# Optimization experiments

Hardware: AMD Instinct MI355X
Metric: run time of the kernel (lower is better)

The kernel has to match this reference:

```python
import jax, jax.numpy as jnp
import numpy as np

S = 7
B = 2
CLS = 20
N = CLS + B * 5  # 30
LAMBDA_COORD = 5.0
LAMBDA_NOOBJ = 0.5
BATCH = 16384


def setup_inputs() -> dict:
    key = jax.random.key(0)
    k1, k2, k3 = jax.random.split(key, 3)
    pred = jax.random.uniform(k1, (BATCH, S, S, N), dtype=jnp.float32)
    target = jax.random.uniform(k2, (BATCH, S, S, N), dtype=jnp.float32)
    # conf channel (index 4) must be exactly 0 or 1 -- it drives the obj/noobj masks
    obj = (jax.random.uniform(k3, (BATCH, S, S)) < 0.15).astype(jnp.float32)
    target = target.at[..., 4].set(obj)
    return {"pred": pred, "target": target}


def _iou(b1, b2):
    # b1: [M, B, 4] xyxy, b2: [M, 4] xyxy -> [M, B]
    lt = jnp.maximum(b1[..., :2], b2[:, None, :2])
    rb = jnp.minimum(b1[..., 2:], b2[:, None, 2:])
    wh = jnp.clip(rb - lt, 0.0)
    inter = wh[..., 0] * wh[..., 1]
    area1 = (b1[..., 2] - b1[..., 0]) * (b1[..., 3] - b1[..., 1])
    area2 = ((b2[:, 2] - b2[:, 0]) * (b2[:, 3] - b2[:, 1]))[:, None]
    union = area1 + area2 - inter
    return jnp.where(union > 0, inter / union, 0.0)


def reference(pred, target):
    batch = pred.shape[0]
    p = pred.reshape(-1, N)   # [M, 30], M = batch*S*S
    t = target.reshape(-1, N)
    obj = (t[:, 4] == 1).astype(pred.dtype)    # positive-cell mask
    noobj = (t[:, 4] == 0).astype(pred.dtype)  # negative-cell mask

    # faithful to source: conf_loc = arange(B)*B + 4 -> [4, 6]
    conf_loc = jnp.arange(B) * B + 4
    noobj_conf_loss = jnp.sum(noobj[:, None] * (p[:, conf_loc] - t[:, conf_loc]) ** 2)

    pb = p[:, : B * 5].reshape(-1, B, 5)  # [M, B, 5] (x, y, w, h, conf)
    tb = t[:, :5]                         # [M, 5] first target box per cell

    # xywh -> xyxy
    pb_xyxy = jnp.concatenate([pb[..., :2] - pb[..., 2:4] / 2,
                               pb[..., :2] + pb[..., 2:4] / 2], axis=-1)
    tb_xyxy = jnp.concatenate([tb[:, :2] - tb[:, 2:4] / 2,
                               tb[:, :2] + tb[:, 2:4] / 2], axis=-1)

    iou = _iou(pb_xyxy, tb_xyxy)                         # [M, B]
    j = jnp.argmax(iou, axis=1)                          # responsible box index
    max_iou = jax.lax.stop_gradient(jnp.max(iou, axis=1))
    resp = jnp.take_along_axis(pb, j[:, None, None], axis=1)[:, 0]  # [M, 5]

    xy_loss = jnp.sum((resp[:, :2] - tb[:, :2]) ** 2, axis=-1)
    wh_loss = jnp.sum((jnp.sqrt(jnp.clip(resp[:, 2:4], 0.0))
                       - jnp.sqrt(jnp.clip(tb[:, 2:4], 0.0))) ** 2, axis=-1)
    coord_loss = jnp.sum(obj * (xy_loss + wh_loss))

    obj_conf_loss = jnp.sum(obj * (resp[:, 4] - max_iou) ** 2)
    class_loss = jnp.sum(obj[:, None] * (p[:, B * 5:] - t[:, B * 5:]) ** 2)

    total = (LAMBDA_COORD * coord_loss + obj_conf_loss
             + LAMBDA_NOOBJ * noobj_conf_loss + class_loss) / batch
    return total
```

## Files before the change

kernel.cpp:

```cpp
#include <hip/hip_runtime.h>


#define TPB 256
#define CELLS 256
#define NPER 30
#define NFLOAT (CELLS * NPER)
#define R_TOTAL (16384 * 7 * 7)
#define NBLOCKS (R_TOTAL / CELLS)

__global__ __launch_bounds__(TPB, 2) void yolo_loss_kernel(
    const float* __restrict__ pred, const float* __restrict__ target,
    float* __restrict__ out)
{
    __shared__ float sp[NFLOAT];
    __shared__ float st[NFLOAT];
    __shared__ float red[TPB / 64];

    const int tid = threadIdx.x;
    const size_t base = (size_t)blockIdx.x * NFLOAT;
    const float* gp = pred + base;
    const float* gt = target + base;

    for (int f = tid * 4; f < NFLOAT; f += TPB * 4) {
        float4 vp = *(const float4*)(gp + f);
        float4 vt = *(const float4*)(gt + f);
        *(float4*)(&sp[f]) = vp;
        *(float4*)(&st[f]) = vt;
    }
    __syncthreads();

    const float* p = &sp[tid * NPER];
    const float* t = &st[tid * NPER];

    float sum = 0.0f;
    const float t4 = t[4];
    if (t4 == 0.0f) {
        float d4 = p[4] - t[4];
        float d6 = p[6] - t[6];
        sum = 0.5f * (d4 * d4 + d6 * d6);
    } else if (t4 == 1.0f) {
        float tx1 = t[0] - t[2] * 0.5f, ty1 = t[1] - t[3] * 0.5f;
        float tx2 = t[0] + t[2] * 0.5f, ty2 = t[1] + t[3] * 0.5f;
        float area2 = (tx2 - tx1) * (ty2 - ty1);
        float iou0, iou1;
        #pragma unroll
        for (int b = 0; b < 2; b++) {
            const float* pb = p + b * 5;
            float x1 = pb[0] - pb[2] * 0.5f, y1 = pb[1] - pb[3] * 0.5f;
            float x2 = pb[0] + pb[2] * 0.5f, y2 = pb[1] + pb[3] * 0.5f;
            float ltx = fmaxf(x1, tx1), lty = fmaxf(y1, ty1);
            float rbx = fminf(x2, tx2), rby = fminf(y2, ty2);
            float w = fmaxf(rbx - ltx, 0.0f), h = fmaxf(rby - lty, 0.0f);
            float inter = w * h;
            float area1 = (x2 - x1) * (y2 - y1);
            float uni = area1 + area2 - inter;
            float iou = (uni > 0.0f) ? (inter / uni) : 0.0f;
            if (b == 0) iou0 = iou; else iou1 = iou;
        }
        int j = (iou1 > iou0) ? 1 : 0;
        float max_iou = fmaxf(iou0, iou1);
        const float* resp = p + j * 5;
        float dx = resp[0] - t[0];
        float dy = resp[1] - t[1];
        float sw = sqrtf(fmaxf(resp[2], 0.0f)) - sqrtf(fmaxf(t[2], 0.0f));
        float sh = sqrtf(fmaxf(resp[3], 0.0f)) - sqrtf(fmaxf(t[3], 0.0f));
        float coord = dx * dx + dy * dy + sw * sw + sh * sh;
        float dc = resp[4] - max_iou;
        float cls = 0.0f;
        #pragma unroll
        for (int k = 10; k < 30; k++) {
            float d = p[k] - t[k];
            cls += d * d;
        }
        sum = 5.0f * coord + dc * dc + cls;
    }

    #pragma unroll
    for (int off = 32; off > 0; off >>= 1)
        sum += __shfl_down(sum, off, 64);
    if ((tid & 63) == 0) red[tid >> 6] = sum;
    __syncthreads();
    if (tid == 0) {
        float s = red[0] + red[1] + red[2] + red[3];
        atomicAdd(out, s * (1.0f / 16384.0f));
    }
}

extern "C" void kernel_launch(void* const* d_in, const int* in_sizes, int n_in,
                              void* d_out, int out_size, void* d_ws, size_t ws_size,
                              hipStream_t stream) {
    const float* pred = (const float*)d_in[0];
    const float* target = (const float*)d_in[1];
    float* out = (float*)d_out;
    hipMemsetAsync(out, 0, sizeof(float), stream);
    yolo_loss_kernel<<<NBLOCKS, TPB, 0, stream>>>(pred, target, out);
}
```

Measured before the change: 213.9 us.

## Load each cell directly into registers instead of staging through LDS

```diff
diff --git a/kernel.cpp b/kernel.cpp
--- a/kernel.cpp
+++ b/kernel.cpp
@@ -2,35 +2,34 @@
 
 
 #define TPB 256
-#define CELLS 256
 #define NPER 30
-#define NFLOAT (CELLS * NPER)
 #define R_TOTAL (16384 * 7 * 7)
-#define NBLOCKS (R_TOTAL / CELLS)
+#define NBLOCKS (R_TOTAL / TPB)
 
-__global__ __launch_bounds__(TPB, 2) void yolo_loss_kernel(
+__global__ __launch_bounds__(TPB, 4) void yolo_loss_kernel(
     const float* __restrict__ pred, const float* __restrict__ target,
     float* __restrict__ out)
 {
-    __shared__ float sp[NFLOAT];
-    __shared__ float st[NFLOAT];
     __shared__ float red[TPB / 64];
 
     const int tid = threadIdx.x;
-    const size_t base = (size_t)blockIdx.x * NFLOAT;
-    const float* gp = pred + base;
-    const float* gt = target + base;
+    const size_t cell = (size_t)blockIdx.x * TPB + tid;
 
-    for (int f = tid * 4; f < NFLOAT; f += TPB * 4) {
-        float4 vp = *(const float4*)(gp + f);
-        float4 vt = *(const float4*)(gt + f);
-        *(float4*)(&sp[f]) = vp;
-        *(float4*)(&st[f]) = vt;
+    float p[NPER], t[NPER];
+    {
+        const float2* gp = (const float2*)(pred + cell * NPER);
+        const float2* gt = (const float2*)(target + cell * NPER);
+        #pragma unroll
+        for (int i = 0; i < NPER / 2; i++) {
+            float2 v = gp[i];
+            p[2 * i] = v.x; p[2 * i + 1] = v.y;
+        }
+        #pragma unroll
+        for (int i = 0; i < NPER / 2; i++) {
+            float2 v = gt[i];
+            t[2 * i] = v.x; t[2 * i + 1] = v.y;
+        }
     }
-    __syncthreads();
-
-    const float* p = &sp[tid * NPER];
-    const float* t = &st[tid * NPER];
 
     float sum = 0.0f;
     const float t4 = t[4];
@@ -42,33 +41,41 @@
         float tx1 = t[0] - t[2] * 0.5f, ty1 = t[1] - t[3] * 0.5f;
         float tx2 = t[0] + t[2] * 0.5f, ty2 = t[1] + t[3] * 0.5f;
         float area2 = (tx2 - tx1) * (ty2 - ty1);
-        float iou0, iou1;
-        #pragma unroll
-        for (int b = 0; b < 2; b++) {
-            const float* pb = p + b * 5;
-            float x1 = pb[0] - pb[2] * 0.5f, y1 = pb[1] - pb[3] * 0.5f;
-            float x2 = pb[0] + pb[2] * 0.5f, y2 = pb[1] + pb[3] * 0.5f;
-            float ltx = fmaxf(x1, tx1), lty = fmaxf(y1, ty1);
-            float rbx = fminf(x2, tx2), rby = fminf(y2, ty2);
-            float w = fmaxf(rbx - ltx, 0.0f), h = fmaxf(rby - lty, 0.0f);
-            float inter = w * h;
-            float area1 = (x2 - x1) * (y2 - y1);
-            float uni = area1 + area2 - inter;
-            float iou = (uni > 0.0f) ? (inter / uni) : 0.0f;
-            if (b == 0) iou0 = iou; else iou1 = iou;
-        }
-        int j = (iou1 > iou0) ? 1 : 0;
+
+        float ax1 = p[0] - p[2] * 0.5f, ay1 = p[1] - p[3] * 0.5f;
+        float ax2 = p[0] + p[2] * 0.5f, ay2 = p[1] + p[3] * 0.5f;
+        float w0 = fmaxf(fminf(ax2, tx2) - fmaxf(ax1, tx1), 0.0f);
+        float h0 = fmaxf(fminf(ay2, ty2) - fmaxf(ay1, ty1), 0.0f);
+        float inter0 = w0 * h0;
+        float uni0 = (ax2 - ax1) * (ay2 - ay1) + area2 - inter0;
+        float iou0 = (uni0 > 0.0f) ? (inter0 / uni0) : 0.0f;
+
+        float bx1 = p[5] - p[7] * 0.5f, by1 = p[6] - p[8] * 0.5f;
+        float bx2 = p[5] + p[7] * 0.5f, by2 = p[6] + p[8] * 0.5f;
+        float w1 = fmaxf(fminf(bx2, tx2) - fmaxf(bx1, tx1), 0.0f);
+        float h1 = fmaxf(fminf(by2, ty2) - fmaxf(by1, ty1), 0.0f);
+        float inter1 = w1 * h1;
+        float uni1 = (bx2 - bx1) * (by2 - by1) + area2 - inter1;
+        float iou1 = (uni1 > 0.0f) ? (inter1 / uni1) : 0.0f;
+
+        bool j1 = (iou1 > iou0);
         float max_iou = fmaxf(iou0, iou1);
-        const float* resp = p + j * 5;
-        float dx = resp[0] - t[0];
-        float dy = resp[1] - t[1];
-        float sw = sqrtf(fmaxf(resp[2], 0.0f)) - sqrtf(fmaxf(t[2], 0.0f));
-        float sh = sqrtf(fmaxf(resp[3], 0.0f)) - sqrtf(fmaxf(t[3], 0.0f));
+        float r0 = j1 ? p[5] : p[0];
+        float r1 = j1 ? p[6] : p[1];
+        float r2 = j1 ? p[7] : p[2];
+        float r3 = j1 ? p[8] : p[3];
+        float r4 = j1 ? p[9] : p[4];
+
+        float dx = r0 - t[0];
+        float dy = r1 - t[1];
+        float sw = sqrtf(fmaxf(r2, 0.0f)) - sqrtf(fmaxf(t[2], 0.0f));
+        float sh = sqrtf(fmaxf(r3, 0.0f)) - sqrtf(fmaxf(t[3], 0.0f));
         float coord = dx * dx + dy * dy + sw * sw + sh * sh;
-        float dc = resp[4] - max_iou;
+        float dc = r4 - max_iou;
+
         float cls = 0.0f;
         #pragma unroll
-        for (int k = 10; k < 30; k++) {
+        for (int k = 10; k < NPER; k++) {
             float d = p[k] - t[k];
             cls += d * d;
         }
```

Measured after the change: 211.4 us. No clear change (-1.2%).
